# Kernel tuning notes

Measured on AMD Instinct MI355X. Metric: run time of the kernel, lower is better.

## Reference

```python
import jax, jax.numpy as jnp
import numpy as np

C = 16          # n_tasks (channels) = num_tasks - 1
NUM_TASKS = 17  # IndexKernel size
RANK = 3        # IndexKernel rank (hard-coded in source)
JITTER = 1e-4
N_MC = 10
N_CLASSES = 10

def _rbf(x1, x2, ls):
    d = (x1[:, None] - x2[None, :]) / ls
    return jnp.exp(-0.5 * d * d)

def _gp_posterior(x, i_tr, y, xs, i_te, c, ls, noise, Btask):
    # Exact GP posterior with Hadamard multitask kernel k(x,x')*B[i,i'].
    T = x.shape[0]
    Kxx = _rbf(x, x, ls) * Btask[i_tr][:, i_tr] + (noise * noise + JITTER) * jnp.eye(T, dtype=x.dtype)
    Ksx = _rbf(xs, x, ls) * Btask[i_te][:, i_tr]
    Kss = _rbf(xs, xs, ls) * Btask[i_te][:, i_te]
    L = jnp.linalg.cholesky(Kxx)
    alpha = jax.scipy.linalg.cho_solve((L, True), y - c)
    mean = c + Ksx @ alpha
    V = jax.scipy.linalg.solve_triangular(L, Ksx.T, lower=True)  # [T, Ts]
    cov = Kss - V.T @ V
    return mean, cov

def _channel_reshape(Z_raw, test_idx):
    # Vectorized version of the triple-loop ragged scatter.
    # Z_raw: [S, B, Ts]; test_idx: [B, Ts] int -> Z: [S, B, max_len, C]
    S, Bb, Ts = Z_raw.shape
    max_len = Ts // C
    onehot = jax.nn.one_hot(test_idx, C, dtype=jnp.int32)                       # [B, Ts, C]
    before = jnp.cumsum(onehot, axis=1) - onehot                                # same-channel count before elem
    pos = jnp.take_along_axis(before, test_idx[..., None], axis=-1)[..., 0]     # [B, Ts]
    b_idx = jnp.broadcast_to(jnp.arange(Bb)[:, None], (Bb, Ts))
    Z = jnp.zeros((S, Bb, max_len, C), Z_raw.dtype)
    return Z.at[:, b_idx, pos, test_idx].set(Z_raw)

def setup_inputs() -> dict:
    key = jax.random.key(0)
    ks = jax.random.split(key, 8)
    B, T, Ts = 32, 1024, 1024
    inputs = jax.random.uniform(ks[0], (B, T, 1), jnp.float32) * 10.0
    indices = jax.random.randint(ks[1], (B, T, 1), 0, C)
    values = jax.random.normal(ks[2], (B, T), jnp.float32)
    test_inputs = jax.random.uniform(ks[3], (B, Ts, 1), jnp.float32) * 10.0
    test_indices = (jnp.arange(Ts, dtype=jnp.int32)[None, :, None] % C) * jnp.ones((B, 1, 1), jnp.int32)
    eps = jax.random.normal(ks[4], (N_MC, B, Ts), jnp.float32)
    mean_const = jnp.zeros((), jnp.float32)
    lengthscale = jnp.ones((), jnp.float32)
    noise = 0.3 * jnp.ones((), jnp.float32)
    W_task = jax.random.normal(ks[5], (NUM_TASKS, RANK), jnp.float32) * 0.3
    v_task = jax.random.uniform(ks[6], (NUM_TASKS,), jnp.float32)
    W_clf = jax.random.normal(ks[7], (C, N_CLASSES), jnp.float32) * 0.1
    b_clf = jnp.zeros((N_CLASSES,), jnp.float32)
    return dict(inputs=inputs, values=values, test_inputs=test_inputs, eps=eps,
                mean_const=mean_const, lengthscale=lengthscale, noise=noise,
                W_task=W_task, v_task=v_task, W_clf=W_clf, b_clf=b_clf,
                indices=indices, test_indices=test_indices)

def reference(inputs, values, test_inputs, eps, mean_const, lengthscale, noise,
              W_task, v_task, W_clf, b_clf, indices, test_indices):
    Btask = W_task @ W_task.T + jnp.diag(jax.nn.softplus(v_task))  # IndexKernel: B = W W^T + diag(v)
    x, xs = inputs[..., 0], test_inputs[..., 0]
    i_tr, i_te = indices[..., 0], test_indices[..., 0]
    mean, cov = jax.vmap(_gp_posterior, in_axes=(0, 0, 0, 0, 0, None, None, None, None))(
        x, i_tr, values, xs, i_te, mean_const, lengthscale, noise, Btask)
    Ts = xs.shape[1]
    Lstar = jnp.linalg.cholesky(cov + JITTER * jnp.eye(Ts, dtype=cov.dtype))
    samples = mean[None] + jnp.einsum('bij,sbj->sbi', Lstar, eps)   # rsample: [S, B, Ts]
    Z = _channel_reshape(samples, i_te)                              # [S, B, max_len, C]
    S, Bb, ml, _ = Z.shape
    Zc = Z.reshape(S * Bb, ml, C)                                    # monte_carlo collapse (flatten(0,1))
    feat = Zc.mean(axis=1)                                           # clf: mean pool + linear
    return feat @ W_clf + b_clf
```

## Files before the change

kernel.cpp:

```cpp
#include <hip/hip_runtime.h>
#include <math.h>

#define TT 1024
#define CH 16
#define SMC 10
#define NCLS 10
#define JIT 1e-4f

__device__ __forceinline__ void tri_map(int tau, int& ti, int& tj) {
    int i = 0, r = tau;
    while (r >= i + 1) { r -= i + 1; i++; }
    ti = i; tj = r;
}

__global__ __launch_bounds__(256) void k_btask(const float* __restrict__ W,
                                               const float* __restrict__ v,
                                               float* __restrict__ Bt) {
    int t = threadIdx.x;
    for (int e = t; e < 17 * 17; e += 256) {
        int i = e / 17, j = e % 17;
        float s = 0.f;
        for (int r = 0; r < 3; r++) s += W[i * 3 + r] * W[j * 3 + r];
        if (i == j) s += log1pf(expf(v[i]));
        Bt[e] = s;
    }
}

__global__ __launch_bounds__(256) void k_build_kxx(const float* __restrict__ x,
                                                   const int* __restrict__ itr,
                                                   const float* __restrict__ lsp,
                                                   const float* __restrict__ noisep,
                                                   const float* __restrict__ Bt,
                                                   float* __restrict__ A, int b0) {
    int bi = blockIdx.x, bj = blockIdx.y, bz = blockIdx.z;
    if (bj > bi) return;
    int b = b0 + bz;
    __shared__ float sxi[128], sxj[128], Btl[289];
    __shared__ int sii[128], sij[128];
    int t = threadIdx.x;
    if (t < 128) { sxi[t] = x[b * TT + bi * 128 + t]; sii[t] = itr[b * TT + bi * 128 + t]; }
    else { int u = t - 128; sxj[u] = x[b * TT + bj * 128 + u]; sij[u] = itr[b * TT + bj * 128 + u]; }
    for (int e = t; e < 289; e += 256) Btl[e] = Bt[e];
    __syncthreads();
    float invls = 1.0f / lsp[0];
    float n2 = noisep[0] * noisep[0] + JIT;
    float* Ab = A + (size_t)bz * TT * TT;
    for (int l = 0; l < 64; l++) {
        int e = l * 256 + t;
        int r = e >> 7, c = e & 127;
        float d = (sxi[r] - sxj[c]) * invls;
        float kv = expf(-0.5f * d * d) * Btl[sii[r] * 17 + sij[c]];
        int gi = bi * 128 + r, gj = bj * 128 + c;
        if (gi == gj) kv += n2;
        Ab[(size_t)gi * TT + gj] = kv;
    }
}

__global__ __launch_bounds__(256) void k_build_g(const float* __restrict__ xs,
                                                 const float* __restrict__ x,
                                                 const int* __restrict__ ite,
                                                 const int* __restrict__ itr,
                                                 const float* __restrict__ lsp,
                                                 const float* __restrict__ Bt,
                                                 float* __restrict__ G, int b0) {
    int bj = blockIdx.x, bi = blockIdx.y, bz = blockIdx.z;
    int b = b0 + bz;
    __shared__ float sxr[128], sxc[128], Btl[289];
    __shared__ int sir[128], sic[128];
    int t = threadIdx.x;
    if (t < 128) { sxr[t] = x[b * TT + bj * 128 + t]; sir[t] = itr[b * TT + bj * 128 + t]; }
    else { int u = t - 128; sxc[u] = xs[b * TT + bi * 128 + u]; sic[u] = ite[b * TT + bi * 128 + u]; }
    for (int e = t; e < 289; e += 256) Btl[e] = Bt[e];
    __syncthreads();
    float invls = 1.0f / lsp[0];
    float* Gb = G + (size_t)bz * TT * TT;
    for (int l = 0; l < 64; l++) {
        int e = l * 256 + t;
        int r = e >> 7, c = e & 127;
        float d = (sxc[c] - sxr[r]) * invls;
        float kv = expf(-0.5f * d * d) * Btl[sic[c] * 17 + sir[r]];
        Gb[(size_t)(bj * 128 + r) * TT + bi * 128 + c] = kv;
    }
}

__global__ __launch_bounds__(256) void k_zinit(const float* __restrict__ values,
                                               const float* __restrict__ mc,
                                               float* __restrict__ zb, int b0) {
    int bz = blockIdx.x, t = threadIdx.x;
    float c0 = mc[0];
    for (int i = t; i < TT; i += 256) zb[bz * TT + i] = values[(size_t)(b0 + bz) * TT + i] - c0;
}

__global__ __launch_bounds__(256) void k_stepA64(float* __restrict__ A,
                                                 float* __restrict__ G,
                                                 float* __restrict__ zb,
                                                 float* __restrict__ Dfac,
                                                 int k, int m, int withG) {
    int bx = blockIdx.x, bz = blockIdx.y;
    float* Ab = A + (size_t)bz * TT * TT;
    float* Gb = G + (size_t)bz * TT * TT;
    int kb = k * 64;
    __shared__ float Ld[64][65];
    __shared__ float WK[64][129];
    __shared__ float invl[64];
    __shared__ float zs[64];
    int t = threadIdx.x;
    for (int l = 0; l < 16; l++) {
        int e = l * 256 + t; int r = e >> 6, c = e & 63;
        Ld[r][c] = Ab[(size_t)(kb + r) * TT + kb + c];
    }
    int jtype = 0, r0 = 0, c0 = 0;
    if (bx >= 1 && bx <= m) {
        jtype = 1; r0 = kb + 64 * bx;
        for (int l = 0; l < 16; l++) {
            int e = l * 256 + t; int r = e >> 6, c = e & 63;
            WK[r][c] = Ab[(size_t)(r0 + r) * TT + kb + c];
        }
    } else if (withG && bx >= m + 1 && bx <= m + 8) {
        jtype = 2; c0 = (bx - m - 1) * 128;
        for (int l = 0; l < 32; l++) {
            int e = l * 256 + t; int r = e >> 7, c = e & 127;
            WK[r][c] = Gb[(size_t)(kb + r) * TT + c0 + c];
        }
    } else if (withG && bx == m + 9) {
        jtype = 3;
        if (t < 64) zs[t] = zb[bz * TT + kb + t];
    }
    __syncthreads();
    for (int j = 0; j < 64; j++) {
        if (t == j) { float d = sqrtf(Ld[j][j]); Ld[j][j] = d; invl[j] = 1.0f / d; }
        __syncthreads();
        float lij = 0.f;
        if (t < 64 && t > j) { lij = Ld[t][j] * invl[j]; Ld[t][j] = lij; }
        __syncthreads();
        if (t < 64 && t > j) {
#pragma unroll 4
            for (int p = j + 1; p <= t; p++) Ld[t][p] -= lij * Ld[p][j];
        }
    }
    __syncthreads();
    if (jtype == 0) {
        if (bx == 0) {
            float* Df = Dfac + ((size_t)bz * 16 + k) * 4096;
            for (int l = 0; l < 16; l++) {
                int e = l * 256 + t; int r = e >> 6, c = e & 63;
                Df[r * 64 + c] = Ld[r][c];
            }
        }
        return;
    }
    if (jtype == 1) {
        if (t < 64) {
            for (int j = 0; j < 64; j++) {
                float xv = WK[t][j] * invl[j];
                WK[t][j] = xv;
#pragma unroll 4
                for (int p = j + 1; p < 64; p++) WK[t][p] -= Ld[p][j] * xv;
            }
        }
        __syncthreads();
        for (int l = 0; l < 16; l++) {
            int e = l * 256 + t; int r = e >> 6, c = e & 63;
            Ab[(size_t)(r0 + r) * TT + kb + c] = WK[r][c];
        }
    } else if (jtype == 2) {
        if (t < 128) {
            for (int j = 0; j < 64; j++) {
                float xv = WK[j][t] * invl[j];
                WK[j][t] = xv;
#pragma unroll 4
                for (int p = j + 1; p < 64; p++) WK[p][t] -= Ld[p][j] * xv;
            }
        }
        __syncthreads();
        for (int l = 0; l < 32; l++) {
            int e = l * 256 + t; int r = e >> 7, c = e & 127;
            Gb[(size_t)(kb + r) * TT + c0 + c] = WK[r][c];
        }
    } else {
        if (t == 0) {
            for (int j = 0; j < 64; j++) {
                float zv = zs[j] * invl[j];
                zs[j] = zv;
#pragma unroll 4
                for (int p = j + 1; p < 64; p++) zs[p] -= Ld[p][j] * zv;
            }
        }
        __syncthreads();
        if (t < 64) zb[bz * TT + kb + t] = zs[t];
    }
}

__global__ __launch_bounds__(256) void k_diagfix64(float* __restrict__ A,
                                                   const float* __restrict__ Dfac) {
    int k = blockIdx.x, bz = blockIdx.y;
    int kb = k * 64;
    float* Ab = A + (size_t)bz * TT * TT;
    const float* Df = Dfac + ((size_t)bz * 16 + k) * 4096;
    int t = threadIdx.x;
    for (int l = 0; l < 16; l++) {
        int e = l * 256 + t; int r = e >> 6, c = e & 63;
        if (c <= r) Ab[(size_t)(kb + r) * TT + kb + c] = Df[r * 64 + c];
    }
}

__global__ __launch_bounds__(256) void k_stepB64(float* __restrict__ A,
                                                 float* __restrict__ G,
                                                 float* __restrict__ zb,
                                                 int k, int m, int bc, int withG) {
    int lin = blockIdx.x;
    int slot = lin & 7, q = lin >> 3;
    int beta = ((slot - 4 * (q & 1)) & 7) + (blockIdx.y << 3);
    if (beta >= bc) return;
    float* Ab = A + (size_t)beta * TT * TT;
    float* Gb = G + (size_t)beta * TT * TT;
    int kb = k * 64;
    int nt = (64 * m + 127) / 128;
    int TL = nt * (nt + 1) / 2;
    __shared__ __align__(16) float At[32][132];
    __shared__ __align__(16) float Bs[32][132];
    __shared__ float zk[64];
    int t = threadIdx.x, tx = t & 15, ty = t >> 4;
    if (q < TL) {
        int ti, tj; tri_map(q, ti, tj);
        int base = kb + 64;
        int r0 = base + ti * 128, c0 = base + tj * 128;
        int rvi = TT - r0; if (rvi > 128) rvi = 128;
        int rvj = TT - c0; if (rvj > 128) rvj = 128;
        float acc[8][8] = {};
        for (int s = 0; s < 2; s++) {
            int k0 = kb + s * 32;
            __syncthreads();
            for (int l = 0; l < 4; l++) {
                int f = l * 256 + t;
                int r = f >> 3, c4 = (f & 7) * 4;
                float4 va = make_float4(0.f, 0.f, 0.f, 0.f), vb = make_float4(0.f, 0.f, 0.f, 0.f);
                if (r < rvi) va = *reinterpret_cast<const float4*>(&Ab[(size_t)(r0 + r) * TT + k0 + c4]);
                if (r < rvj) vb = *reinterpret_cast<const float4*>(&Ab[(size_t)(c0 + r) * TT + k0 + c4]);
                At[c4 + 0][r] = va.x; At[c4 + 1][r] = va.y; At[c4 + 2][r] = va.z; At[c4 + 3][r] = va.w;
                Bs[c4 + 0][r] = vb.x; Bs[c4 + 1][r] = vb.y; Bs[c4 + 2][r] = vb.z; Bs[c4 + 3][r] = vb.w;
            }
            __syncthreads();
#pragma unroll 4
            for (int p = 0; p < 32; p++) {
                float4 a0 = *reinterpret_cast<const float4*>(&At[p][ty * 8]);
                float4 a1 = *reinterpret_cast<const float4*>(&At[p][ty * 8 + 4]);
                float4 b0 = *reinterpret_cast<const float4*>(&Bs[p][tx * 4]);
                float4 b1 = *reinterpret_cast<const float4*>(&Bs[p][tx * 4 + 64]);
                float aa[8] = {a0.x, a0.y, a0.z, a0.w, a1.x, a1.y, a1.z, a1.w};
                float bl[4] = {b0.x, b0.y, b0.z, b0.w};
                float bh[4] = {b1.x, b1.y, b1.z, b1.w};
                for (int i = 0; i < 8; i++) {
                    for (int j = 0; j < 4; j++) acc[i][j] += aa[i] * bl[j];
                    for (int j = 0; j < 4; j++) acc[i][j + 4] += aa[i] * bh[j];
                }
            }
        }
        if (tx * 4 >= rvj) return;
        for (int i = 0; i < 8; i++) {
            int rr = ty * 8 + i;
            if (rr >= rvi) break;
            float* cp0 = &Ab[(size_t)(r0 + rr) * TT + c0 + tx * 4];
            float4 cv0 = *reinterpret_cast<float4*>(cp0);
            cv0.x -= acc[i][0]; cv0.y -= acc[i][1]; cv0.z -= acc[i][2]; cv0.w -= acc[i][3];
            *reinterpret_cast<float4*>(cp0) = cv0;
            if (rvj > 64) {
                float* cp1 = cp0 + 64;
                float4 cv1 = *reinterpret_cast<float4*>(cp1);
                cv1.x -= acc[i][4]; cv1.y -= acc[i][5]; cv1.z -= acc[i][6]; cv1.w -= acc[i][7];
                *reinterpret_cast<float4*>(cp1) = cv1;
            }
        }
        return;
    }
    int e = q - TL;
    int ti = e / 9, sub = e % 9;
    int r0 = kb + 64 + ti * 128;
    int rvi = TT - r0; if (rvi > 128) rvi = 128;
    if (sub < 8) {
        int c0 = sub * 128;
        float acc[8][8] = {};
        for (int s = 0; s < 2; s++) {
            int k0 = kb + s * 32;
            __syncthreads();
            for (int l = 0; l < 4; l++) {
                int f = l * 256 + t;
                int r = f >> 3, c4 = (f & 7) * 4;
                float4 va = make_float4(0.f, 0.f, 0.f, 0.f);
                if (r < rvi) va = *reinterpret_cast<const float4*>(&Ab[(size_t)(r0 + r) * TT + k0 + c4]);
                At[c4 + 0][r] = va.x; At[c4 + 1][r] = va.y; At[c4 + 2][r] = va.z; At[c4 + 3][r] = va.w;
                int kr = f >> 5, cc4 = (f & 31) * 4;
                float4 vb = *reinterpret_cast<const float4*>(&Gb[(size_t)(k0 + kr) * TT + c0 + cc4]);
                *reinterpret_cast<float4*>(&Bs[kr][cc4]) = vb;
            }
            __syncthreads();
#pragma unroll 4
            for (int p = 0; p < 32; p++) {
                float4 a0 = *reinterpret_cast<const float4*>(&At[p][ty * 8]);
                float4 a1 = *reinterpret_cast<const float4*>(&At[p][ty * 8 + 4]);
                float4 b0 = *reinterpret_cast<const float4*>(&Bs[p][tx * 4]);
                float4 b1 = *reinterpret_cast<const float4*>(&Bs[p][tx * 4 + 64]);
                float aa[8] = {a0.x, a0.y, a0.z, a0.w, a1.x, a1.y, a1.z, a1.w};
                float bl[4] = {b0.x, b0.y, b0.z, b0.w};
                float bh[4] = {b1.x, b1.y, b1.z, b1.w};
                for (int i = 0; i < 8; i++) {
                    for (int j = 0; j < 4; j++) acc[i][j] += aa[i] * bl[j];
                    for (int j = 0; j < 4; j++) acc[i][j + 4] += aa[i] * bh[j];
                }
            }
        }
        for (int i = 0; i < 8; i++) {
            int rr = ty * 8 + i;
            if (rr >= rvi) break;
            float* cp0 = &Gb[(size_t)(r0 + rr) * TT + c0 + tx * 4];
            float4 cv0 = *reinterpret_cast<float4*>(cp0);
            cv0.x -= acc[i][0]; cv0.y -= acc[i][1]; cv0.z -= acc[i][2]; cv0.w -= acc[i][3];
            *reinterpret_cast<float4*>(cp0) = cv0;
            float* cp1 = cp0 + 64;
            float4 cv1 = *reinterpret_cast<float4*>(cp1);
            cv1.x -= acc[i][4]; cv1.y -= acc[i][5]; cv1.z -= acc[i][6]; cv1.w -= acc[i][7];
            *reinterpret_cast<float4*>(cp1) = cv1;
        }
    } else {
        if (t < 64) zk[t] = zb[beta * TT + kb + t];
        float accz = 0.f;
        for (int s = 0; s < 2; s++) {
            int k0 = kb + s * 32;
            __syncthreads();
            for (int l = 0; l < 4; l++) {
                int f = l * 256 + t;
                int r = f >> 3, c4 = (f & 7) * 4;
                float4 va = make_float4(0.f, 0.f, 0.f, 0.f);
                if (r < rvi) va = *reinterpret_cast<const float4*>(&Ab[(size_t)(r0 + r) * TT + k0 + c4]);
                At[c4 + 0][r] = va.x; At[c4 + 1][r] = va.y; At[c4 + 2][r] = va.z; At[c4 + 3][r] = va.w;
            }
            __syncthreads();
            if (t < 128) {
                for (int qq = 0; qq < 32; qq++) accz += At[qq][t] * zk[s * 32 + qq];
            }
        }
        if (t < rvi) zb[beta * TT + r0 + t] -= accz;
    }
}

__global__ __launch_bounds__(256) void k_mean(const float* __restrict__ G,
                                              const float* __restrict__ zb,
                                              const float* __restrict__ mc,
                                              float* __restrict__ meanb, int b0) {
    int bz = blockIdx.y; int b = b0 + bz;
    const float* Gb = G + (size_t)bz * TT * TT;
    int i = blockIdx.x * 256 + threadIdx.x;
    float acc = 0.f;
    for (int j = 0; j < TT; j++) acc += Gb[(size_t)j * TT + i] * zb[bz * TT + j];
    meanb[b * TT + i] = mc[0] + acc;
}

__global__ __launch_bounds__(256) void k_cov128(const float* __restrict__ G,
                                                const float* __restrict__ xs,
                                                const int* __restrict__ ite,
                                                const float* __restrict__ lsp,
                                                const float* __restrict__ Bt,
                                                float* __restrict__ A, int b0, int bc) {
    int lin = blockIdx.x;
    int slot = lin & 7, tau = lin >> 3;
    int beta = ((slot - 4 * (tau & 1)) & 7) + (blockIdx.y << 3);
    if (beta >= bc) return;
    int ti, tj; tri_map(tau, ti, tj);
    int b = b0 + beta;
    const float* Gb = G + (size_t)beta * TT * TT;
    float* Ab = A + (size_t)beta * TT * TT;
    int i0 = ti * 128, j0 = tj * 128;
    __shared__ __align__(16) float Va[32][132];
    __shared__ __align__(16) float Vb[32][132];
    __shared__ float sxi[128], sxj[128], Btl[289];
    __shared__ int sei[128], sej[128];
    int t = threadIdx.x, tx = t & 15, ty = t >> 4;
    if (t < 128) { sxi[t] = xs[b * TT + i0 + t]; sei[t] = ite[b * TT + i0 + t]; }
    else { int u = t - 128; sxj[u] = xs[b * TT + j0 + u]; sej[u] = ite[b * TT + j0 + u]; }
    for (int e = t; e < 289; e += 256) Btl[e] = Bt[e];
    float acc[8][8] = {};
    for (int k0 = 0; k0 < TT; k0 += 32) {
        __syncthreads();
        for (int l = 0; l < 4; l++) {
            int f = l * 256 + t;
            int kr = f >> 5, cc4 = (f & 31) * 4;
            *reinterpret_cast<float4*>(&Va[kr][cc4]) =
                *reinterpret_cast<const float4*>(&Gb[(size_t)(k0 + kr) * TT + i0 + cc4]);
            *reinterpret_cast<float4*>(&Vb[kr][cc4]) =
                *reinterpret_cast<const float4*>(&Gb[(size_t)(k0 + kr) * TT + j0 + cc4]);
        }
        __syncthreads();
#pragma unroll 4
        for (int p = 0; p < 32; p++) {
            float4 a0 = *reinterpret_cast<const float4*>(&Va[p][ty * 8]);
            float4 a1 = *reinterpret_cast<const float4*>(&Va[p][ty * 8 + 4]);
            float4 b0 = *reinterpret_cast<const float4*>(&Vb[p][tx * 4]);
            float4 b1 = *reinterpret_cast<const float4*>(&Vb[p][tx * 4 + 64]);
            float aa[8] = {a0.x, a0.y, a0.z, a0.w, a1.x, a1.y, a1.z, a1.w};
            float bl[4] = {b0.x, b0.y, b0.z, b0.w};
            float bh[4] = {b1.x, b1.y, b1.z, b1.w};
            for (int i = 0; i < 8; i++) {
                for (int j = 0; j < 4; j++) acc[i][j] += aa[i] * bl[j];
                for (int j = 0; j < 4; j++) acc[i][j + 4] += aa[i] * bh[j];
            }
        }
    }
    float invls = 1.0f / lsp[0];
    for (int i = 0; i < 8; i++) {
        int ri = ty * 8 + i; int gi = i0 + ri;
        float xi = sxi[ri]; int ci = sei[ri] * 17;
        float vo[8];
        for (int j = 0; j < 4; j++) {
            int rj = tx * 4 + j; int gj = j0 + rj;
            float d = (xi - sxj[rj]) * invls;
            float v = expf(-0.5f * d * d) * Btl[ci + sej[rj]] - acc[i][j];
            if (gi == gj) v += JIT;
            vo[j] = v;
        }
        for (int j = 0; j < 4; j++) {
            int rj = 64 + tx * 4 + j; int gj = j0 + rj;
            float d = (xi - sxj[rj]) * invls;
            float v = expf(-0.5f * d * d) * Btl[ci + sej[rj]] - acc[i][j + 4];
            if (gi == gj) v += JIT;
            vo[j + 4] = v;
        }
        float* cp = &Ab[(size_t)gi * TT + j0 + tx * 4];
        *reinterpret_cast<float4*>(cp) = make_float4(vo[0], vo[1], vo[2], vo[3]);
        *reinterpret_cast<float4*>(cp + 64) = make_float4(vo[4], vo[5], vo[6], vo[7]);
    }
}

__global__ __launch_bounds__(256) void k_P(const float* __restrict__ A,
                                           const int* __restrict__ ite,
                                           float* __restrict__ P, int b0) {
    int bz = blockIdx.y; int b = b0 + bz;
    const float* Ab = A + (size_t)bz * TT * TT;
    __shared__ int chl[TT];
    __shared__ float accl[CH * 256];
    int t = threadIdx.x;
    for (int i = t; i < TT; i += 256) chl[i] = ite[b * TT + i];
    for (int c = 0; c < CH; c++) accl[c * 256 + t] = 0.f;
    __syncthreads();
    int j0 = blockIdx.x * 256;
    int j = j0 + t;
    for (int i = j0; i < TT; i++) {
        float v = Ab[(size_t)i * TT + j];
        if (i >= j) accl[chl[i] * 256 + t] += v;
    }
    for (int c = 0; c < CH; c++) P[((size_t)b * CH + c) * TT + j] = accl[c * 256 + t];
}

__global__ __launch_bounds__(64) void k_msum(const float* __restrict__ meanb,
                                             const int* __restrict__ ite,
                                             float* __restrict__ msum, int b0) {
    int bz = blockIdx.x; int b = b0 + bz;
    __shared__ float pacc[CH][65];
    int t = threadIdx.x;
    for (int c = 0; c < CH; c++) pacc[c][t] = 0.f;
    __syncthreads();
    for (int i = t; i < TT; i += 64) pacc[ite[b * TT + i]][t] += meanb[b * TT + i];
    __syncthreads();
    if (t < CH) {
        float s = 0.f;
        for (int u = 0; u < 64; u++) s += pacc[t][u];
        msum[b * CH + t] = s;
    }
}

__global__ __launch_bounds__(256) void k_featout(const float* __restrict__ P,
                                                 const float* __restrict__ msum,
                                                 const float* __restrict__ eps,
                                                 const float* __restrict__ Wc,
                                                 const float* __restrict__ bc_,
                                                 float* __restrict__ out, int b0, int Btot) {
    int s = blockIdx.x; int b = b0 + blockIdx.y;
    __shared__ float el[TT];
    __shared__ float part[256];
    __shared__ float featl[CH];
    int t = threadIdx.x;
    for (int i = t; i < TT; i += 256) el[i] = eps[((size_t)s * Btot + b) * TT + i];
    __syncthreads();
    int c = t >> 4, seg = t & 15;
    float acc = 0.f;
    const float* Pr = &P[((size_t)b * CH + c) * TT + seg * 64];
    for (int j = 0; j < 64; j++) acc += Pr[j] * el[seg * 64 + j];
    part[t] = acc;
    __syncthreads();
    if (t < CH) {
        float s2 = msum[b * CH + t];
        for (int g = 0; g < 16; g++) s2 += part[t * 16 + g];
        featl[t] = s2 * (1.0f / 64.0f);
    }
    __syncthreads();
    if (t < NCLS) {
        float o = bc_[t];
        for (int c2 = 0; c2 < CH; c2++) o += featl[c2] * Wc[c2 * NCLS + t];
        out[((size_t)s * Btot + b) * NCLS + t] = o;
    }
}

extern "C" void kernel_launch(void* const* d_in, const int* in_sizes, int n_in,
                              void* d_out, int out_size, void* d_ws, size_t ws_size,
                              hipStream_t stream) {
    const float* inputs       = (const float*)d_in[0];
    const float* values       = (const float*)d_in[1];
    const float* test_inputs  = (const float*)d_in[2];
    const float* eps          = (const float*)d_in[3];
    const float* mc           = (const float*)d_in[4];
    const float* ls           = (const float*)d_in[5];
    const float* noise        = (const float*)d_in[6];
    const float* W_task       = (const float*)d_in[7];
    const float* v_task       = (const float*)d_in[8];
    const float* W_clf        = (const float*)d_in[9];
    const float* b_clf        = (const float*)d_in[10];
    const int*   indices      = (const int*)d_in[11];
    const int*   test_indices = (const int*)d_in[12];
    float* out = (float*)d_out;

    int Btot = in_sizes[1] / TT;

    float* ws = (float*)d_ws;
    size_t off = 0;
    float* Bt    = ws + off; off += 512;
    float* zbuf  = ws + off; off += (size_t)Btot * TT;
    float* meanb = ws + off; off += (size_t)Btot * TT;
    float* Pb    = ws + off; off += (size_t)Btot * CH * TT;
    float* msum  = ws + off; off += (size_t)Btot * CH;
    off = (off + 63) & ~(size_t)63;

    size_t avail = (ws_size / 4 > off) ? (ws_size / 4 - off) : 0;
    size_t per = 2 * (size_t)TT * TT + 16 * 4096;
    int chunk = (int)(avail / per);
    if (chunk < 1) chunk = 1;
    if (chunk > Btot) chunk = Btot;
    float* bigA = ws + off;
    float* bigG = bigA + (size_t)chunk * TT * TT;
    float* Dfac = bigG + (size_t)chunk * TT * TT;

    k_btask<<<1, 256, 0, stream>>>(W_task, v_task, Bt);

    for (int b0 = 0; b0 < Btot; b0 += chunk) {
        int bcc = chunk; if (b0 + bcc > Btot) bcc = Btot - b0;
        int by = (bcc + 7) / 8;

        k_build_kxx<<<dim3(8, 8, bcc), 256, 0, stream>>>(inputs, indices, ls, noise, Bt, bigA, b0);
        k_build_g<<<dim3(8, 8, bcc), 256, 0, stream>>>(test_inputs, inputs, test_indices, indices, ls, Bt, bigG, b0);
        k_zinit<<<bcc, 256, 0, stream>>>(values, mc, zbuf, b0);
        for (int k = 0; k < 16; k++) {
            int m = 15 - k;
            k_stepA64<<<dim3(m + 10, bcc), 256, 0, stream>>>(bigA, bigG, zbuf, Dfac, k, m, 1);
            int nt = (64 * m + 127) / 128;
            int Q = nt * (nt + 1) / 2 + nt * 9;
            if (m > 0) k_stepB64<<<dim3(Q * 8, by), 256, 0, stream>>>(bigA, bigG, zbuf, k, m, bcc, 1);
        }
        k_mean<<<dim3(4, bcc), 256, 0, stream>>>(bigG, zbuf, mc, meanb, b0);
        k_cov128<<<dim3(36 * 8, by), 256, 0, stream>>>(bigG, test_inputs, test_indices, ls, Bt, bigA, b0, bcc);
        for (int k = 0; k < 16; k++) {
            int m = 15 - k;
            k_stepA64<<<dim3(m + 1, bcc), 256, 0, stream>>>(bigA, bigA, zbuf, Dfac, k, m, 0);
            int nt = (64 * m + 127) / 128;
            int Q = nt * (nt + 1) / 2;
            if (m > 0) k_stepB64<<<dim3(Q * 8, by), 256, 0, stream>>>(bigA, bigA, zbuf, k, m, bcc, 0);
        }
        k_diagfix64<<<dim3(16, bcc), 256, 0, stream>>>(bigA, Dfac);
        k_P<<<dim3(4, bcc), 256, 0, stream>>>(bigA, test_indices, Pb, b0);
        k_msum<<<bcc, 64, 0, stream>>>(meanb, test_indices, msum, b0);
        k_featout<<<dim3(SMC, bcc), 256, 0, stream>>>(Pb, msum, eps, W_clf, b_clf, out, b0, Btot);
    }
}
```

Measured before the change: 10.28 ms.

## Fuse blocked Cholesky step launches into persistent kernel with per-batch grid barriers

Replaces the 32 per-step kernel launches (panel factor/solve and trailing update) of each blocked Cholesky with a single persistent kernel per factorization. Each batch item gets 16 workgroups that loop over the 16 block steps and synchronize through an atomic counter/generation barrier in global memory. This removes launch overhead and inter-kernel gaps. In exchange every workgroup redundantly factors the diagonal block, each step's work is spread over only 16 workgroups, and the software barrier risks deadlock if not all workgroups are co-resident.

```diff
diff --git a/kernel.cpp b/kernel.cpp
--- a/kernel.cpp
+++ b/kernel.cpp
@@ -6,11 +6,30 @@
 #define SMC 10
 #define NCLS 10
 #define JIT 1e-4f
+#define NBLK 16
 
 __device__ __forceinline__ void tri_map(int tau, int& ti, int& tj) {
     int i = 0, r = tau;
     while (r >= i + 1) { r -= i + 1; i++; }
     ti = i; tj = r;
+}
+
+__device__ __forceinline__ void bbar(unsigned* cnt, unsigned* gen) {
+    __syncthreads();
+    if (threadIdx.x == 0) {
+        __threadfence();
+        unsigned g = __hip_atomic_load(gen, __ATOMIC_ACQUIRE, __HIP_MEMORY_SCOPE_AGENT);
+        unsigned a = __hip_atomic_fetch_add(cnt, 1u, __ATOMIC_ACQ_REL, __HIP_MEMORY_SCOPE_AGENT) + 1u;
+        if (a == (unsigned)NBLK) {
+            __hip_atomic_store(cnt, 0u, __ATOMIC_RELEASE, __HIP_MEMORY_SCOPE_AGENT);
+            __hip_atomic_fetch_add(gen, 1u, __ATOMIC_ACQ_REL, __HIP_MEMORY_SCOPE_AGENT);
+        } else {
+            while (__hip_atomic_load(gen, __ATOMIC_ACQUIRE, __HIP_MEMORY_SCOPE_AGENT) == g)
+                __builtin_amdgcn_s_sleep(2);
+        }
+        __threadfence();
+    }
+    __syncthreads();
 }
 
 __global__ __launch_bounds__(256) void k_btask(const float* __restrict__ W,
@@ -91,103 +110,251 @@
     for (int i = t; i < TT; i += 256) zb[bz * TT + i] = values[(size_t)(b0 + bz) * TT + i] - c0;
 }
 
-__global__ __launch_bounds__(256) void k_stepA64(float* __restrict__ A,
-                                                 float* __restrict__ G,
-                                                 float* __restrict__ zb,
-                                                 float* __restrict__ Dfac,
-                                                 int k, int m, int withG) {
-    int bx = blockIdx.x, bz = blockIdx.y;
-    float* Ab = A + (size_t)bz * TT * TT;
-    float* Gb = G + (size_t)bz * TT * TT;
-    int kb = k * 64;
-    __shared__ float Ld[64][65];
-    __shared__ float WK[64][129];
-    __shared__ float invl[64];
-    __shared__ float zs[64];
-    int t = threadIdx.x;
-    for (int l = 0; l < 16; l++) {
-        int e = l * 256 + t; int r = e >> 6, c = e & 63;
-        Ld[r][c] = Ab[(size_t)(kb + r) * TT + kb + c];
-    }
-    int jtype = 0, r0 = 0, c0 = 0;
-    if (bx >= 1 && bx <= m) {
-        jtype = 1; r0 = kb + 64 * bx;
-        for (int l = 0; l < 16; l++) {
-            int e = l * 256 + t; int r = e >> 6, c = e & 63;
-            WK[r][c] = Ab[(size_t)(r0 + r) * TT + kb + c];
-        }
-    } else if (withG && bx >= m + 1 && bx <= m + 8) {
-        jtype = 2; c0 = (bx - m - 1) * 128;
-        for (int l = 0; l < 32; l++) {
-            int e = l * 256 + t; int r = e >> 7, c = e & 127;
-            WK[r][c] = Gb[(size_t)(kb + r) * TT + c0 + c];
-        }
-    } else if (withG && bx == m + 9) {
-        jtype = 3;
-        if (t < 64) zs[t] = zb[bz * TT + kb + t];
-    }
-    __syncthreads();
-    for (int j = 0; j < 64; j++) {
-        if (t == j) { float d = sqrtf(Ld[j][j]); Ld[j][j] = d; invl[j] = 1.0f / d; }
-        __syncthreads();
-        float lij = 0.f;
-        if (t < 64 && t > j) { lij = Ld[t][j] * invl[j]; Ld[t][j] = lij; }
-        __syncthreads();
-        if (t < 64 && t > j) {
-#pragma unroll 4
-            for (int p = j + 1; p <= t; p++) Ld[t][p] -= lij * Ld[p][j];
-        }
-    }
-    __syncthreads();
-    if (jtype == 0) {
-        if (bx == 0) {
-            float* Df = Dfac + ((size_t)bz * 16 + k) * 4096;
+__global__ __launch_bounds__(256) void k_chain(float* __restrict__ A,
+                                               float* __restrict__ G,
+                                               float* __restrict__ zb,
+                                               float* __restrict__ Dfac,
+                                               unsigned* __restrict__ bars,
+                                               int bc, int withG) {
+    int bid = blockIdx.x;
+    int slot = bid & 7;
+    int grp = bid >> 3;
+    int i = grp & (NBLK - 1);
+    int beta = slot + 8 * (grp >> 4);
+    if (beta >= bc) return;
+    float* Ab = A + (size_t)beta * TT * TT;
+    float* Gb = G + (size_t)beta * TT * TT;
+    unsigned* cnt = bars + beta * 2;
+    unsigned* gen = cnt + 1;
+
+    __shared__ __align__(16) float smem[12416];
+    __shared__ float invl[64], zvec[64], zk[64];
+    float (*Ld)[65]  = reinterpret_cast<float (*)[65]>(smem);
+    float (*WK)[129] = reinterpret_cast<float (*)[129]>(smem + 4160);
+    float (*At)[132] = reinterpret_cast<float (*)[132]>(smem);
+    float (*Bs)[132] = reinterpret_cast<float (*)[132]>(smem + 4224);
+    int t = threadIdx.x, tx = t & 15, ty = t >> 4;
+
+    for (int k = 0; k < 16; k++) {
+        int kb = k * 64, m = 15 - k;
+        int njA = m + (withG ? 9 : 0);
+        bool needF = (i == 0) || (i < njA);
+        if (needF) {
             for (int l = 0; l < 16; l++) {
                 int e = l * 256 + t; int r = e >> 6, c = e & 63;
-                Df[r * 64 + c] = Ld[r][c];
+                Ld[r][c] = Ab[(size_t)(kb + r) * TT + kb + c];
             }
-        }
-        return;
-    }
-    if (jtype == 1) {
-        if (t < 64) {
+            __syncthreads();
             for (int j = 0; j < 64; j++) {
-                float xv = WK[t][j] * invl[j];
-                WK[t][j] = xv;
-#pragma unroll 4
-                for (int p = j + 1; p < 64; p++) WK[t][p] -= Ld[p][j] * xv;
+                if (t == j) { float d = sqrtf(Ld[j][j]); Ld[j][j] = d; invl[j] = 1.0f / d; }
+                __syncthreads();
+                float lij = 0.f;
+                if (t < 64 && t > j) { lij = Ld[t][j] * invl[j]; Ld[t][j] = lij; }
+                __syncthreads();
+                if (t < 64 && t > j) {
+#pragma unroll 4
+                    for (int p = j + 1; p <= t; p++) Ld[t][p] -= lij * Ld[p][j];
+                }
             }
-        }
-        __syncthreads();
-        for (int l = 0; l < 16; l++) {
-            int e = l * 256 + t; int r = e >> 6, c = e & 63;
-            Ab[(size_t)(r0 + r) * TT + kb + c] = WK[r][c];
-        }
-    } else if (jtype == 2) {
-        if (t < 128) {
-            for (int j = 0; j < 64; j++) {
-                float xv = WK[j][t] * invl[j];
-                WK[j][t] = xv;
-#pragma unroll 4
-                for (int p = j + 1; p < 64; p++) WK[p][t] -= Ld[p][j] * xv;
+            __syncthreads();
+            if (i == 0) {
+                float* Df = Dfac + ((size_t)beta * 16 + k) * 4096;
+                for (int l = 0; l < 16; l++) {
+                    int e = l * 256 + t; int r = e >> 6, c = e & 63;
+                    Df[r * 64 + c] = Ld[r][c];
+                }
             }
-        }
-        __syncthreads();
-        for (int l = 0; l < 32; l++) {
-            int e = l * 256 + t; int r = e >> 7, c = e & 127;
-            Gb[(size_t)(kb + r) * TT + c0 + c] = WK[r][c];
-        }
-    } else {
-        if (t == 0) {
-            for (int j = 0; j < 64; j++) {
-                float zv = zs[j] * invl[j];
-                zs[j] = zv;
-#pragma unroll 4
-                for (int p = j + 1; p < 64; p++) zs[p] -= Ld[p][j] * zv;
+            for (int j = i; j < njA; j += NBLK) {
+                if (j < m) {
+                    int r0 = kb + 64 * (j + 1);
+                    __syncthreads();
+                    for (int l = 0; l < 16; l++) {
+                        int e = l * 256 + t; int r = e >> 6, c = e & 63;
+                        WK[r][c] = Ab[(size_t)(r0 + r) * TT + kb + c];
+                    }
+                    __syncthreads();
+                    if (t < 64) {
+                        for (int jj = 0; jj < 64; jj++) {
+                            float xv = WK[t][jj] * invl[jj];
+                            WK[t][jj] = xv;
+#pragma unroll 4
+                            for (int p = jj + 1; p < 64; p++) WK[t][p] -= Ld[p][jj] * xv;
+                        }
+                    }
+                    __syncthreads();
+                    for (int l = 0; l < 16; l++) {
+                        int e = l * 256 + t; int r = e >> 6, c = e & 63;
+                        Ab[(size_t)(r0 + r) * TT + kb + c] = WK[r][c];
+                    }
+                } else if (j < m + 8) {
+                    int c0 = (j - m) * 128;
+                    __syncthreads();
+                    for (int l = 0; l < 32; l++) {
+                        int e = l * 256 + t; int r = e >> 7, c = e & 127;
+                        WK[r][c] = Gb[(size_t)(kb + r) * TT + c0 + c];
+                    }
+                    __syncthreads();
+                    if (t < 128) {
+                        for (int jj = 0; jj < 64; jj++) {
+                            float xv = WK[jj][t] * invl[jj];
+                            WK[jj][t] = xv;
+#pragma unroll 4
+                            for (int p = jj + 1; p < 64; p++) WK[p][t] -= Ld[p][jj] * xv;
+                        }
+                    }
+                    __syncthreads();
+                    for (int l = 0; l < 32; l++) {
+                        int e = l * 256 + t; int r = e >> 7, c = e & 127;
+                        Gb[(size_t)(kb + r) * TT + c0 + c] = WK[r][c];
+                    }
+                } else {
+                    __syncthreads();
+                    if (t < 64) zvec[t] = zb[beta * TT + kb + t];
+                    __syncthreads();
+                    if (t == 0) {
+                        for (int jj = 0; jj < 64; jj++) {
+                            float zv = zvec[jj] * invl[jj];
+                            zvec[jj] = zv;
+#pragma unroll 4
+                            for (int p = jj + 1; p < 64; p++) zvec[p] -= Ld[p][jj] * zv;
+                        }
+                    }
+                    __syncthreads();
+                    if (t < 64) zb[beta * TT + kb + t] = zvec[t];
+                }
             }
         }
-        __syncthreads();
-        if (t < 64) zb[bz * TT + kb + t] = zs[t];
+        bbar(cnt, gen);
+        if (m > 0) {
+            int nt = (64 * m + 127) / 128;
+            int TL = nt * (nt + 1) / 2;
+            int nq = TL + (withG ? nt * 9 : 0);
+            for (int q = i; q < nq; q += NBLK) {
+                if (q < TL) {
+                    int ti_, tj_; tri_map(q, ti_, tj_);
+                    int base = kb + 64;
+                    int r0 = base + ti_ * 128, c0 = base + tj_ * 128;
+                    int rvi = TT - r0; if (rvi > 128) rvi = 128;
+                    int rvj = TT - c0; if (rvj > 128) rvj = 128;
+                    float acc[8][8] = {};
+                    for (int s = 0; s < 2; s++) {
+                        int k0 = kb + s * 32;
+                        __syncthreads();
+                        for (int l = 0; l < 4; l++) {
+                            int f = l * 256 + t;
+                            int r = f >> 3, c4 = (f & 7) * 4;
+                            float4 va = make_float4(0.f, 0.f, 0.f, 0.f), vb = make_float4(0.f, 0.f, 0.f, 0.f);
+                            if (r < rvi) va = *reinterpret_cast<const float4*>(&Ab[(size_t)(r0 + r) * TT + k0 + c4]);
+                            if (r < rvj) vb = *reinterpret_cast<const float4*>(&Ab[(size_t)(c0 + r) * TT + k0 + c4]);
+                            At[c4 + 0][r] = va.x; At[c4 + 1][r] = va.y; At[c4 + 2][r] = va.z; At[c4 + 3][r] = va.w;
+                            Bs[c4 + 0][r] = vb.x; Bs[c4 + 1][r] = vb.y; Bs[c4 + 2][r] = vb.z; Bs[c4 + 3][r] = vb.w;
+                        }
+                        __syncthreads();
+#pragma unroll 4
+                        for (int p = 0; p < 32; p++) {
+                            float4 a0 = *reinterpret_cast<const float4*>(&At[p][ty * 8]);
+                            float4 a1 = *reinterpret_cast<const float4*>(&At[p][ty * 8 + 4]);
+                            float4 b0 = *reinterpret_cast<const float4*>(&Bs[p][tx * 4]);
+                            float4 b1 = *reinterpret_cast<const float4*>(&Bs[p][tx * 4 + 64]);
+                            float aa[8] = {a0.x, a0.y, a0.z, a0.w, a1.x, a1.y, a1.z, a1.w};
+                            float bl[4] = {b0.x, b0.y, b0.z, b0.w};
+                            float bh[4] = {b1.x, b1.y, b1.z, b1.w};
+                            for (int ii = 0; ii < 8; ii++) {
+                                for (int jj = 0; jj < 4; jj++) acc[ii][jj] += aa[ii] * bl[jj];
+                                for (int jj = 0; jj < 4; jj++) acc[ii][jj + 4] += aa[ii] * bh[jj];
+                            }
+                        }
+                    }
+                    if (tx * 4 < rvj) {
+                        for (int ii = 0; ii < 8; ii++) {
+                            int rr = ty * 8 + ii;
+                            if (rr >= rvi) break;
+                            float* cp0 = &Ab[(size_t)(r0 + rr) * TT + c0 + tx * 4];
+                            float4 cv0 = *reinterpret_cast<float4*>(cp0);
+                            cv0.x -= acc[ii][0]; cv0.y -= acc[ii][1]; cv0.z -= acc[ii][2]; cv0.w -= acc[ii][3];
+                            *reinterpret_cast<float4*>(cp0) = cv0;
+                            if (rvj > 64) {
+                                float* cp1 = cp0 + 64;
+                                float4 cv1 = *reinterpret_cast<float4*>(cp1);
+                                cv1.x -= acc[ii][4]; cv1.y -= acc[ii][5]; cv1.z -= acc[ii][6]; cv1.w -= acc[ii][7];
+                                *reinterpret_cast<float4*>(cp1) = cv1;
+                            }
+                        }
+                    }
+                } else {
+                    int e = q - TL;
+                    int ti_ = e / 9, sub = e % 9;
+                    int r0 = kb + 64 + ti_ * 128;
+                    int rvi = TT - r0; if (rvi > 128) rvi = 128;
+                    if (sub < 8) {
+                        int c0 = sub * 128;
+                        float acc[8][8] = {};
+                        for (int s = 0; s < 2; s++) {
+                            int k0 = kb + s * 32;
+                            __syncthreads();
+                            for (int l = 0; l < 4; l++) {
+                                int f = l * 256 + t;
+                                int r = f >> 3, c4 = (f & 7) * 4;
+                                float4 va = make_float4(0.f, 0.f, 0.f, 0.f);
+                                if (r < rvi) va = *reinterpret_cast<const float4*>(&Ab[(size_t)(r0 + r) * TT + k0 + c4]);
+                                At[c4 + 0][r] = va.x; At[c4 + 1][r] = va.y; At[c4 + 2][r] = va.z; At[c4 + 3][r] = va.w;
+                                int kr = f >> 5, cc4 = (f & 31) * 4;
+                                float4 vb = *reinterpret_cast<const float4*>(&Gb[(size_t)(k0 + kr) * TT + c0 + cc4]);
+                                *reinterpret_cast<float4*>(&Bs[kr][cc4]) = vb;
+                            }
+                            __syncthreads();
+#pragma unroll 4
+                            for (int p = 0; p < 32; p++) {
+                                float4 a0 = *reinterpret_cast<const float4*>(&At[p][ty * 8]);
+                                float4 a1 = *reinterpret_cast<const float4*>(&At[p][ty * 8 + 4]);
+                                float4 b0 = *reinterpret_cast<const float4*>(&Bs[p][tx * 4]);
+                                float4 b1 = *reinterpret_cast<const float4*>(&Bs[p][tx * 4 + 64]);
+                                float aa[8] = {a0.x, a0.y, a0.z, a0.w, a1.x, a1.y, a1.z, a1.w};
+                                float bl[4] = {b0.x, b0.y, b0.z, b0.w};
+                                float bh[4] = {b1.x, b1.y, b1.z, b1.w};
+                                for (int ii = 0; ii < 8; ii++) {
+                                    for (int jj = 0; jj < 4; jj++) acc[ii][jj] += aa[ii] * bl[jj];
+                                    for (int jj = 0; jj < 4; jj++) acc[ii][jj + 4] += aa[ii] * bh[jj];
+                                }
+                            }
+                        }
+                        for (int ii = 0; ii < 8; ii++) {
+                            int rr = ty * 8 + ii;
+                            if (rr >= rvi) break;
+                            float* cp0 = &Gb[(size_t)(r0 + rr) * TT + c0 + tx * 4];
+                            float4 cv0 = *reinterpret_cast<float4*>(cp0);
+                            cv0.x -= acc[ii][0]; cv0.y -= acc[ii][1]; cv0.z -= acc[ii][2]; cv0.w -= acc[ii][3];
+                            *reinterpret_cast<float4*>(cp0) = cv0;
+                            float* cp1 = cp0 + 64;
+                            float4 cv1 = *reinterpret_cast<float4*>(cp1);
+                            cv1.x -= acc[ii][4]; cv1.y -= acc[ii][5]; cv1.z -= acc[ii][6]; cv1.w -= acc[ii][7];
+                            *reinterpret_cast<float4*>(cp1) = cv1;
+                        }
+                    } else {
+                        __syncthreads();
+                        if (t < 64) zk[t] = zb[beta * TT + kb + t];
+                        float accz = 0.f;
+                        for (int s = 0; s < 2; s++) {
+                            int k0 = kb + s * 32;
+                            __syncthreads();
+                            for (int l = 0; l < 4; l++) {
+                                int f = l * 256 + t;
+                                int r = f >> 3, c4 = (f & 7) * 4;
+                                float4 va = make_float4(0.f, 0.f, 0.f, 0.f);
+                                if (r < rvi) va = *reinterpret_cast<const float4*>(&Ab[(size_t)(r0 + r) * TT + k0 + c4]);
+                                At[c4 + 0][r] = va.x; At[c4 + 1][r] = va.y; At[c4 + 2][r] = va.z; At[c4 + 3][r] = va.w;
+                            }
+                            __syncthreads();
+                            if (t < 128) {
+                                for (int qq = 0; qq < 32; qq++) accz += At[qq][t] * zk[s * 32 + qq];
+                            }
+                        }
+                        if (t < rvi) zb[beta * TT + r0 + t] -= accz;
+                    }
+                }
+            }
+        }
+        if (k < 15) bbar(cnt, gen);
     }
 }
 
@@ -201,145 +368,6 @@
     for (int l = 0; l < 16; l++) {
         int e = l * 256 + t; int r = e >> 6, c = e & 63;
         if (c <= r) Ab[(size_t)(kb + r) * TT + kb + c] = Df[r * 64 + c];
-    }
-}
-
-__global__ __launch_bounds__(256) void k_stepB64(float* __restrict__ A,
-                                                 float* __restrict__ G,
-                                                 float* __restrict__ zb,
-                                                 int k, int m, int bc, int withG) {
-    int lin = blockIdx.x;
-    int slot = lin & 7, q = lin >> 3;
-    int beta = ((slot - 4 * (q & 1)) & 7) + (blockIdx.y << 3);
-    if (beta >= bc) return;
-    float* Ab = A + (size_t)beta * TT * TT;
-    float* Gb = G + (size_t)beta * TT * TT;
-    int kb = k * 64;
-    int nt = (64 * m + 127) / 128;
-    int TL = nt * (nt + 1) / 2;
-    __shared__ __align__(16) float At[32][132];
-    __shared__ __align__(16) float Bs[32][132];
-    __shared__ float zk[64];
-    int t = threadIdx.x, tx = t & 15, ty = t >> 4;
-    if (q < TL) {
-        int ti, tj; tri_map(q, ti, tj);
-        int base = kb + 64;
-        int r0 = base + ti * 128, c0 = base + tj * 128;
-        int rvi = TT - r0; if (rvi > 128) rvi = 128;
-        int rvj = TT - c0; if (rvj > 128) rvj = 128;
-        float acc[8][8] = {};
-        for (int s = 0; s < 2; s++) {
-            int k0 = kb + s * 32;
-            __syncthreads();
-            for (int l = 0; l < 4; l++) {
-                int f = l * 256 + t;
-                int r = f >> 3, c4 = (f & 7) * 4;
-                float4 va = make_float4(0.f, 0.f, 0.f, 0.f), vb = make_float4(0.f, 0.f, 0.f, 0.f);
-                if (r < rvi) va = *reinterpret_cast<const float4*>(&Ab[(size_t)(r0 + r) * TT + k0 + c4]);
-                if (r < rvj) vb = *reinterpret_cast<const float4*>(&Ab[(size_t)(c0 + r) * TT + k0 + c4]);
-                At[c4 + 0][r] = va.x; At[c4 + 1][r] = va.y; At[c4 + 2][r] = va.z; At[c4 + 3][r] = va.w;
-                Bs[c4 + 0][r] = vb.x; Bs[c4 + 1][r] = vb.y; Bs[c4 + 2][r] = vb.z; Bs[c4 + 3][r] = vb.w;
-            }
-            __syncthreads();
-#pragma unroll 4
-            for (int p = 0; p < 32; p++) {
-                float4 a0 = *reinterpret_cast<const float4*>(&At[p][ty * 8]);
-                float4 a1 = *reinterpret_cast<const float4*>(&At[p][ty * 8 + 4]);
-                float4 b0 = *reinterpret_cast<const float4*>(&Bs[p][tx * 4]);
-                float4 b1 = *reinterpret_cast<const float4*>(&Bs[p][tx * 4 + 64]);
-                float aa[8] = {a0.x, a0.y, a0.z, a0.w, a1.x, a1.y, a1.z, a1.w};
-                float bl[4] = {b0.x, b0.y, b0.z, b0.w};
-                float bh[4] = {b1.x, b1.y, b1.z, b1.w};
-                for (int i = 0; i < 8; i++) {
-                    for (int j = 0; j < 4; j++) acc[i][j] += aa[i] * bl[j];
-                    for (int j = 0; j < 4; j++) acc[i][j + 4] += aa[i] * bh[j];
-                }
-            }
-        }
-        if (tx * 4 >= rvj) return;
-        for (int i = 0; i < 8; i++) {
-            int rr = ty * 8 + i;
-            if (rr >= rvi) break;
-            float* cp0 = &Ab[(size_t)(r0 + rr) * TT + c0 + tx * 4];
-            float4 cv0 = *reinterpret_cast<float4*>(cp0);
-            cv0.x -= acc[i][0]; cv0.y -= acc[i][1]; cv0.z -= acc[i][2]; cv0.w -= acc[i][3];
-            *reinterpret_cast<float4*>(cp0) = cv0;
-            if (rvj > 64) {
-                float* cp1 = cp0 + 64;
-                float4 cv1 = *reinterpret_cast<float4*>(cp1);
-                cv1.x -= acc[i][4]; cv1.y -= acc[i][5]; cv1.z -= acc[i][6]; cv1.w -= acc[i][7];
-                *reinterpret_cast<float4*>(cp1) = cv1;
-            }
-        }
-        return;
-    }
-    int e = q - TL;
-    int ti = e / 9, sub = e % 9;
-    int r0 = kb + 64 + ti * 128;
-    int rvi = TT - r0; if (rvi > 128) rvi = 128;
-    if (sub < 8) {
-        int c0 = sub * 128;
-        float acc[8][8] = {};
-        for (int s = 0; s < 2; s++) {
-            int k0 = kb + s * 32;
-            __syncthreads();
-            for (int l = 0; l < 4; l++) {
-                int f = l * 256 + t;
-                int r = f >> 3, c4 = (f & 7) * 4;
-                float4 va = make_float4(0.f, 0.f, 0.f, 0.f);
-                if (r < rvi) va = *reinterpret_cast<const float4*>(&Ab[(size_t)(r0 + r) * TT + k0 + c4]);
-                At[c4 + 0][r] = va.x; At[c4 + 1][r] = va.y; At[c4 + 2][r] = va.z; At[c4 + 3][r] = va.w;
-                int kr = f >> 5, cc4 = (f & 31) * 4;
-                float4 vb = *reinterpret_cast<const float4*>(&Gb[(size_t)(k0 + kr) * TT + c0 + cc4]);
-                *reinterpret_cast<float4*>(&Bs[kr][cc4]) = vb;
-            }
-            __syncthreads();
-#pragma unroll 4
-            for (int p = 0; p < 32; p++) {
-                float4 a0 = *reinterpret_cast<const float4*>(&At[p][ty * 8]);
-                float4 a1 = *reinterpret_cast<const float4*>(&At[p][ty * 8 + 4]);
-                float4 b0 = *reinterpret_cast<const float4*>(&Bs[p][tx * 4]);
-                float4 b1 = *reinterpret_cast<const float4*>(&Bs[p][tx * 4 + 64]);
-                float aa[8] = {a0.x, a0.y, a0.z, a0.w, a1.x, a1.y, a1.z, a1.w};
-                float bl[4] = {b0.x, b0.y, b0.z, b0.w};
-                float bh[4] = {b1.x, b1.y, b1.z, b1.w};
-                for (int i = 0; i < 8; i++) {
-                    for (int j = 0; j < 4; j++) acc[i][j] += aa[i] * bl[j];
-                    for (int j = 0; j < 4; j++) acc[i][j + 4] += aa[i] * bh[j];
-                }
-            }
-        }
-        for (int i = 0; i < 8; i++) {
-            int rr = ty * 8 + i;
-            if (rr >= rvi) break;
-            float* cp0 = &Gb[(size_t)(r0 + rr) * TT + c0 + tx * 4];
-            float4 cv0 = *reinterpret_cast<float4*>(cp0);
-            cv0.x -= acc[i][0]; cv0.y -= acc[i][1]; cv0.z -= acc[i][2]; cv0.w -= acc[i][3];
-            *reinterpret_cast<float4*>(cp0) = cv0;
-            float* cp1 = cp0 + 64;
-            float4 cv1 = *reinterpret_cast<float4*>(cp1);
-            cv1.x -= acc[i][4]; cv1.y -= acc[i][5]; cv1.z -= acc[i][6]; cv1.w -= acc[i][7];
-            *reinterpret_cast<float4*>(cp1) = cv1;
-        }
-    } else {
-        if (t < 64) zk[t] = zb[beta * TT + kb + t];
-        float accz = 0.f;
-        for (int s = 0; s < 2; s++) {
-            int k0 = kb + s * 32;
-            __syncthreads();
-            for (int l = 0; l < 4; l++) {
-                int f = l * 256 + t;
-                int r = f >> 3, c4 = (f & 7) * 4;
-                float4 va = make_float4(0.f, 0.f, 0.f, 0.f);
-                if (r < rvi) va = *reinterpret_cast<const float4*>(&Ab[(size_t)(r0 + r) * TT + k0 + c4]);
-                At[c4 + 0][r] = va.x; At[c4 + 1][r] = va.y; At[c4 + 2][r] = va.z; At[c4 + 3][r] = va.w;
-            }
-            __syncthreads();
-            if (t < 128) {
-                for (int qq = 0; qq < 32; qq++) accz += At[qq][t] * zk[s * 32 + qq];
-            }
-        }
-        if (t < rvi) zb[beta * TT + r0 + t] -= accz;
     }
 }
 
@@ -521,6 +549,7 @@
 
     float* ws = (float*)d_ws;
     size_t off = 0;
+    unsigned* bars = (unsigned*)ws; off += 64;
     float* Bt    = ws + off; off += 512;
     float* zbuf  = ws + off; off += (size_t)Btot * TT;
     float* meanb = ws + off; off += (size_t)Btot * TT;
@@ -537,31 +566,21 @@
     float* bigG = bigA + (size_t)chunk * TT * TT;
     float* Dfac = bigG + (size_t)chunk * TT * TT;
 
+    hipMemsetAsync(bars, 0, 256, stream);
     k_btask<<<1, 256, 0, stream>>>(W_task, v_task, Bt);
 
     for (int b0 = 0; b0 < Btot; b0 += chunk) {
         int bcc = chunk; if (b0 + bcc > Btot) bcc = Btot - b0;
         int by = (bcc + 7) / 8;
+        int gx = 8 * NBLK * by;
 
         k_build_kxx<<<dim3(8, 8, bcc), 256, 0, stream>>>(inputs, indices, ls, noise, Bt, bigA, b0);
         k_build_g<<<dim3(8, 8, bcc), 256, 0, stream>>>(test_inputs, inputs, test_indices, indices, ls, Bt, bigG, b0);
         k_zinit<<<bcc, 256, 0, stream>>>(values, mc, zbuf, b0);
-        for (int k = 0; k < 16; k++) {
-            int m = 15 - k;
-            k_stepA64<<<dim3(m + 10, bcc), 256, 0, stream>>>(bigA, bigG, zbuf, Dfac, k, m, 1);
-            int nt = (64 * m + 127) / 128;
-            int Q = nt * (nt + 1) / 2 + nt * 9;
-            if (m > 0) k_stepB64<<<dim3(Q * 8, by), 256, 0, stream>>>(bigA, bigG, zbuf, k, m, bcc, 1);
-        }
+        k_chain<<<gx, 256, 0, stream>>>(bigA, bigG, zbuf, Dfac, bars, bcc, 1);
         k_mean<<<dim3(4, bcc), 256, 0, stream>>>(bigG, zbuf, mc, meanb, b0);
         k_cov128<<<dim3(36 * 8, by), 256, 0, stream>>>(bigG, test_inputs, test_indices, ls, Bt, bigA, b0, bcc);
-        for (int k = 0; k < 16; k++) {
-            int m = 15 - k;
-            k_stepA64<<<dim3(m + 1, bcc), 256, 0, stream>>>(bigA, bigA, zbuf, Dfac, k, m, 0);
-            int nt = (64 * m + 127) / 128;
-            int Q = nt * (nt + 1) / 2;
-            if (m > 0) k_stepB64<<<dim3(Q * 8, by), 256, 0, stream>>>(bigA, bigA, zbuf, k, m, bcc, 0);
-        }
+        k_chain<<<gx, 256, 0, stream>>>(bigA, bigA, zbuf, Dfac, bars, bcc, 0);
         k_diagfix64<<<dim3(16, bcc), 256, 0, stream>>>(bigA, Dfac);
         k_P<<<dim3(4, bcc), 256, 0, stream>>>(bigA, test_indices, Pb, b0);
         k_msum<<<bcc, 64, 0, stream>>>(meanb, test_indices, msum, b0);
```

Result: slower. 26.71 ms (median of 4 runs) (+159.7%).

## Shrink covariance tiles to 64 and fuse mean computation into diagonal tiles

Applied to the files above, without the earlier changes.

Replaces the 128x128-tile covariance SYRK kernel with a 64x64-tile version launched over 136 lower-triangle tiles per batch, so each thread holds a 4x4 accumulator and more blocks run at once. The separate mean kernel is removed: diagonal tiles reuse the G panel already in shared memory to compute G^T z for their rows and write the posterior mean. Smaller tiles lower register pressure and give more parallelism, but they double global reads of G per unit of work and leave the extra mean work on diagonal blocks only.

```diff
diff --git a/kernel.cpp b/kernel.cpp
--- a/kernel.cpp
+++ b/kernel.cpp
@@ -343,24 +343,16 @@
     }
 }
 
-__global__ __launch_bounds__(256) void k_mean(const float* __restrict__ G,
-                                              const float* __restrict__ zb,
-                                              const float* __restrict__ mc,
-                                              float* __restrict__ meanb, int b0) {
-    int bz = blockIdx.y; int b = b0 + bz;
-    const float* Gb = G + (size_t)bz * TT * TT;
-    int i = blockIdx.x * 256 + threadIdx.x;
-    float acc = 0.f;
-    for (int j = 0; j < TT; j++) acc += Gb[(size_t)j * TT + i] * zb[bz * TT + j];
-    meanb[b * TT + i] = mc[0] + acc;
-}
-
-__global__ __launch_bounds__(256) void k_cov128(const float* __restrict__ G,
-                                                const float* __restrict__ xs,
-                                                const int* __restrict__ ite,
-                                                const float* __restrict__ lsp,
-                                                const float* __restrict__ Bt,
-                                                float* __restrict__ A, int b0, int bc) {
+__global__ __launch_bounds__(256) void k_cov64(const float* __restrict__ G,
+                                               const float* __restrict__ xs,
+                                               const int* __restrict__ ite,
+                                               const float* __restrict__ lsp,
+                                               const float* __restrict__ Bt,
+                                               float* __restrict__ A,
+                                               const float* __restrict__ zb,
+                                               const float* __restrict__ mc,
+                                               float* __restrict__ meanb,
+                                               int b0, int bc) {
     int lin = blockIdx.x;
     int slot = lin & 7, tau = lin >> 3;
     int beta = ((slot - 4 * (tau & 1)) & 7) + (blockIdx.y << 3);
@@ -369,47 +361,54 @@
     int b = b0 + beta;
     const float* Gb = G + (size_t)beta * TT * TT;
     float* Ab = A + (size_t)beta * TT * TT;
-    int i0 = ti * 128, j0 = tj * 128;
-    __shared__ __align__(16) float Va[32][132];
-    __shared__ __align__(16) float Vb[32][132];
-    __shared__ float sxi[128], sxj[128], Btl[289];
-    __shared__ int sei[128], sej[128];
+    int i0 = ti * 64, j0 = tj * 64;
+    __shared__ __align__(16) float Va[32][68];
+    __shared__ __align__(16) float Vb[32][68];
+    __shared__ float sxi[64], sxj[64], Btl[289], zs[32];
+    __shared__ int sei[64], sej[64];
     int t = threadIdx.x, tx = t & 15, ty = t >> 4;
-    if (t < 128) { sxi[t] = xs[b * TT + i0 + t]; sei[t] = ite[b * TT + i0 + t]; }
-    else { int u = t - 128; sxj[u] = xs[b * TT + j0 + u]; sej[u] = ite[b * TT + j0 + u]; }
+    if (t < 64) { sxi[t] = xs[b * TT + i0 + t]; sei[t] = ite[b * TT + i0 + t]; }
+    else if (t < 128) { int u = t - 64; sxj[u] = xs[b * TT + j0 + u]; sej[u] = ite[b * TT + j0 + u]; }
     for (int e = t; e < 289; e += 256) Btl[e] = Bt[e];
-    float acc[8][8] = {};
+    bool diag = (ti == tj);
+    float acc[4][4] = {};
+    float macc[4] = {0.f, 0.f, 0.f, 0.f};
     for (int k0 = 0; k0 < TT; k0 += 32) {
         __syncthreads();
-        for (int l = 0; l < 4; l++) {
+        for (int l = 0; l < 2; l++) {
             int f = l * 256 + t;
-            int kr = f >> 5, cc4 = (f & 31) * 4;
+            int kr = f >> 4, cc4 = (f & 15) * 4;
             *reinterpret_cast<float4*>(&Va[kr][cc4]) =
                 *reinterpret_cast<const float4*>(&Gb[(size_t)(k0 + kr) * TT + i0 + cc4]);
             *reinterpret_cast<float4*>(&Vb[kr][cc4]) =
                 *reinterpret_cast<const float4*>(&Gb[(size_t)(k0 + kr) * TT + j0 + cc4]);
         }
+        if (diag && t < 32) zs[t] = zb[beta * TT + k0 + t];
         __syncthreads();
 #pragma unroll 4
         for (int p = 0; p < 32; p++) {
-            float4 a0 = *reinterpret_cast<const float4*>(&Va[p][ty * 8]);
-            float4 a1 = *reinterpret_cast<const float4*>(&Va[p][ty * 8 + 4]);
-            float4 b0 = *reinterpret_cast<const float4*>(&Vb[p][tx * 4]);
-            float4 b1 = *reinterpret_cast<const float4*>(&Vb[p][tx * 4 + 64]);
-            float aa[8] = {a0.x, a0.y, a0.z, a0.w, a1.x, a1.y, a1.z, a1.w};
-            float bl[4] = {b0.x, b0.y, b0.z, b0.w};
-            float bh[4] = {b1.x, b1.y, b1.z, b1.w};
-            for (int i = 0; i < 8; i++) {
-                for (int j = 0; j < 4; j++) acc[i][j] += aa[i] * bl[j];
-                for (int j = 0; j < 4; j++) acc[i][j + 4] += aa[i] * bh[j];
+            float4 av = *reinterpret_cast<const float4*>(&Va[p][ty * 4]);
+            float4 bv = *reinterpret_cast<const float4*>(&Vb[p][tx * 4]);
+            float aa[4] = {av.x, av.y, av.z, av.w};
+            float bb[4] = {bv.x, bv.y, bv.z, bv.w};
+            for (int i = 0; i < 4; i++)
+                for (int j = 0; j < 4; j++) acc[i][j] += aa[i] * bb[j];
+        }
+        if (diag && ty == 0) {
+#pragma unroll 4
+            for (int p = 0; p < 32; p++) {
+                float zv = zs[p];
+                float4 av = *reinterpret_cast<const float4*>(&Va[p][tx * 4]);
+                macc[0] += av.x * zv; macc[1] += av.y * zv;
+                macc[2] += av.z * zv; macc[3] += av.w * zv;
             }
         }
     }
     float invls = 1.0f / lsp[0];
-    for (int i = 0; i < 8; i++) {
-        int ri = ty * 8 + i; int gi = i0 + ri;
+    for (int i = 0; i < 4; i++) {
+        int ri = ty * 4 + i; int gi = i0 + ri;
         float xi = sxi[ri]; int ci = sei[ri] * 17;
-        float vo[8];
+        float vo[4];
         for (int j = 0; j < 4; j++) {
             int rj = tx * 4 + j; int gj = j0 + rj;
             float d = (xi - sxj[rj]) * invls;
@@ -417,16 +416,13 @@
             if (gi == gj) v += JIT;
             vo[j] = v;
         }
-        for (int j = 0; j < 4; j++) {
-            int rj = 64 + tx * 4 + j; int gj = j0 + rj;
-            float d = (xi - sxj[rj]) * invls;
-            float v = expf(-0.5f * d * d) * Btl[ci + sej[rj]] - acc[i][j + 4];
-            if (gi == gj) v += JIT;
-            vo[j + 4] = v;
-        }
-        float* cp = &Ab[(size_t)gi * TT + j0 + tx * 4];
-        *reinterpret_cast<float4*>(cp) = make_float4(vo[0], vo[1], vo[2], vo[3]);
-        *reinterpret_cast<float4*>(cp + 64) = make_float4(vo[4], vo[5], vo[6], vo[7]);
+        *reinterpret_cast<float4*>(&Ab[(size_t)gi * TT + j0 + tx * 4]) =
+            make_float4(vo[0], vo[1], vo[2], vo[3]);
+    }
+    if (diag && ty == 0) {
+        float c0 = mc[0];
+        for (int j = 0; j < 4; j++)
+            meanb[(size_t)b * TT + i0 + tx * 4 + j] = c0 + macc[j];
     }
 }
 
@@ -553,8 +549,8 @@
             int Q = nt * (nt + 1) / 2 + nt * 9;
             if (m > 0) k_stepB64<<<dim3(Q * 8, by), 256, 0, stream>>>(bigA, bigG, zbuf, k, m, bcc, 1);
         }
-        k_mean<<<dim3(4, bcc), 256, 0, stream>>>(bigG, zbuf, mc, meanb, b0);
-        k_cov128<<<dim3(36 * 8, by), 256, 0, stream>>>(bigG, test_inputs, test_indices, ls, Bt, bigA, b0, bcc);
+        k_cov64<<<dim3(136 * 8, by), 256, 0, stream>>>(bigG, test_inputs, test_indices, ls, Bt,
+                                                       bigA, zbuf, mc, meanb, b0, bcc);
         for (int k = 0; k < 16; k++) {
             int m = 15 - k;
             k_stepA64<<<dim3(m + 1, bcc), 256, 0, stream>>>(bigA, bigA, zbuf, Dfac, k, m, 0);
```

Measured after the change: 10.14 ms. No clear change (-1.4%).
